# Optimization experiments

Measured on AMD Instinct MI355X. Metric: run time of the kernel, lower is better.

Reference implementation:

```python
import jax, jax.numpy as jnp
import numpy as np

N, CT, L = 8, 1024, 1024
HEADS, GROUPS = 16, 8
BN_EPS = 1e-5


def conv_bn(x, w, b, gamma, beta, mean, var, groups):
    # 1x1 grouped Conv1d followed by eval-mode BatchNorm1d.
    # x: [N, Cin, L], w: [Cout, Cin//groups], b: [Cout]
    n, cin, l = x.shape
    cout = w.shape[0]
    xg = x.reshape(n, groups, cin // groups, l)
    wg = w.reshape(groups, cout // groups, cin // groups)
    y = jnp.einsum('goi,ngil->ngol', wg, xg).reshape(n, cout, l) + b[None, :, None]
    inv = gamma / jnp.sqrt(var + BN_EPS)
    return y * inv[None, :, None] + (beta - mean * inv)[None, :, None]


def _make_params(key, cout, cin_per_group):
    ks = jax.random.split(key, 4)
    w = jax.random.normal(ks[0], (cout, cin_per_group), jnp.float32) * 0.02
    b = jnp.zeros((cout,), jnp.float32)
    gamma = jnp.ones((cout,), jnp.float32)
    beta = jnp.zeros((cout,), jnp.float32)
    mean = jax.random.normal(ks[1], (cout,), jnp.float32) * 0.1
    var = jax.random.uniform(ks[2], (cout,), jnp.float32, 0.5, 1.5)
    return w, b, gamma, beta, mean, var


def setup_inputs() -> dict:
    key = jax.random.key(0)
    k0, k1, k2, k3, k4 = jax.random.split(key, 5)
    tokens = jax.random.normal(k0, (N, CT, L), jnp.float32)
    out = {'tokens': tokens}
    for name, kk, cout, cpg in [
        ('k', k1, CT // 2, CT // GROUPS),
        ('q', k2, CT // 2, CT // GROUPS),
        ('v', k3, CT, CT // GROUPS),
        ('f', k4, CT, CT),  # ff_conv: groups=1
    ]:
        w, b, g, be, m, v = _make_params(kk, cout, cpg)
        out[f'{name}_w'], out[f'{name}_b'] = w, b
        out[f'{name}_gamma'], out[f'{name}_beta'] = g, be
        out[f'{name}_mean'], out[f'{name}_var'] = m, v
    return out


def reference(tokens,
              k_w, k_b, k_gamma, k_beta, k_mean, k_var,
              q_w, q_b, q_gamma, q_beta, q_mean, q_var,
              v_w, v_b, v_gamma, v_beta, v_mean, v_var,
              f_w, f_b, f_gamma, f_beta, f_mean, f_var):
    n, ct, l = tokens.shape
    h = HEADS
    k = conv_bn(tokens, k_w, k_b, k_gamma, k_beta, k_mean, k_var, GROUPS).reshape(n, h, ct // 2 // h, l)
    q = conv_bn(tokens, q_w, q_b, q_gamma, q_beta, q_mean, q_var, GROUPS).reshape(n, h, ct // 2 // h, l)
    v = conv_bn(tokens, v_w, v_b, v_gamma, v_beta, v_mean, v_var, GROUPS).reshape(n, h, ct // h, l)
    # kq = k^T q : [n, h, L_k, L_q]; NOTE original scales by sqrt(kq.size(2)) = sqrt(L)
    kq = jnp.einsum('nhdk,nhdq->nhkq', k, q)
    att = jax.nn.softmax(kq / jnp.sqrt(jnp.asarray(l, tokens.dtype)), axis=2)
    kqv = jnp.einsum('nhdk,nhkq->nhdq', v, att).reshape(n, ct, l)
    tokens = tokens + kqv
    tokens = tokens + conv_bn(tokens, f_w, f_b, f_gamma, f_beta, f_mean, f_var, 1)
    return tokens
```

## Files before the change

### kernel.cpp

```cpp
#include <hip/hip_runtime.h>
#include <hip/hip_bf16.h>
#include <math.h>

#define NB 8
#define BN_EPS 1e-5f
#define CEXP 0.04508422002778011f

typedef __attribute__((ext_vector_type(4))) float f32x4;
typedef __attribute__((ext_vector_type(8))) short short8;

__device__ __forceinline__ float bf2f(ushort h) {
    union { unsigned u; float f; } v; v.u = ((unsigned)h) << 16;
    return v.f;
}
__device__ __forceinline__ ushort f2bfu(float f) {
    __hip_bfloat16 h = __float2bfloat16(f);
    union { __hip_bfloat16 h; ushort u; } c; c.h = h; return c.u;
}
__device__ __forceinline__ void gld16(const ushort* g, ushort* l) {
    __builtin_amdgcn_global_load_lds(
        (const __attribute__((address_space(1))) void*)g,
        (__attribute__((address_space(3))) void*)l, 16, 0, 0);
}

#define O_WKQV   0u
#define O_BKQV   524288u
#define O_WFH    532480u
#define O_WFL    2629632u
#define O_BF     4726784u
#define O_TOKT   4730880u
#define O_T2TL   21508096u
#define O_KT     38285312u
#define O_QT     46673920u
#define O_V      55062528u
#define O_T2     71839744u

__global__ void prep_kqv(
    const float* __restrict__ kw, const float* __restrict__ kb, const float* __restrict__ kg,
    const float* __restrict__ kbe, const float* __restrict__ km, const float* __restrict__ kv,
    const float* __restrict__ qw, const float* __restrict__ qb, const float* __restrict__ qg,
    const float* __restrict__ qbe, const float* __restrict__ qm, const float* __restrict__ qv,
    const float* __restrict__ vw, const float* __restrict__ vb, const float* __restrict__ vg,
    const float* __restrict__ vbe, const float* __restrict__ vm, const float* __restrict__ vv,
    ushort* __restrict__ wf, float* __restrict__ bf)
{
    int idx = blockIdx.x * blockDim.x + threadIdx.x;
    int co = idx >> 7, ci = idx & 127;
    const float *w, *b, *g, *be, *m, *vr; int r;
    if (co < 512)       { w = kw; b = kb; g = kg; be = kbe; m = km; vr = kv; r = co; }
    else if (co < 1024) { w = qw; b = qb; g = qg; be = qbe; m = qm; vr = qv; r = co - 512; }
    else                { w = vw; b = vb; g = vg; be = vbe; m = vm; vr = vv; r = co - 1024; }
    float inv = g[r] * rsqrtf(vr[r] + BN_EPS);
    wf[idx] = f2bfu(w[r * 128 + ci] * inv);
    if (ci == 0) bf[co] = (b[r] - m[r]) * inv + be[r];
}

__global__ void prep_f(
    const float* __restrict__ fw, const float* __restrict__ fb, const float* __restrict__ fg,
    const float* __restrict__ fbe, const float* __restrict__ fm, const float* __restrict__ fv,
    ushort* __restrict__ wfh, ushort* __restrict__ wfl, float* __restrict__ bf)
{
    int idx = blockIdx.x * blockDim.x + threadIdx.x;
    int co = idx >> 10, ci = idx & 1023;
    float inv = fg[co] * rsqrtf(fv[co] + BN_EPS);
    float w = fw[idx] * inv;
    ushort hi = f2bfu(w);
    wfh[idx] = hi;
    wfl[idx] = f2bfu(w - bf2f(hi));
    if (ci == 0) bf[co] = (fb[co] - fm[co]) * inv + fbe[co];
}

__global__ __launch_bounds__(256) void transpose_tokens(
    const float* __restrict__ x, ushort* __restrict__ xt)
{
    __shared__ float Ts[64][68];
    const int l0 = blockIdx.x * 64, c0 = blockIdx.y * 64, n = blockIdx.z;
    const int tid = threadIdx.x;
    #pragma unroll
    for (int r = 0; r < 4; ++r) {
        int idx = tid + 256 * r;
        int ci = idx >> 4, li4 = (idx & 15) * 4;
        float4 v4 = *(const float4*)&x[((size_t)(n * 1024 + c0 + ci)) * 1024 + l0 + li4];
        *(float4*)&Ts[ci][li4] = v4;
    }
    __syncthreads();
    #pragma unroll
    for (int r = 0; r < 2; ++r) {
        int idx = tid + 256 * r;
        int lr = idx >> 3, oc = idx & 7;
        union { ushort u[8]; uint4 v; } pk;
        #pragma unroll
        for (int i = 0; i < 8; ++i) pk.u[i] = f2bfu(Ts[oc * 8 + i][lr]);
        *(uint4*)&xt[((size_t)(n * 1024 + l0 + lr)) * 1024 + c0 + oc * 8] = pk.v;
    }
}

__global__ __launch_bounds__(256) void conv_kqv_mfma(
    const ushort* __restrict__ xt, const ushort* __restrict__ wq,
    const float* __restrict__ bq,
    ushort* __restrict__ KT, ushort* __restrict__ QT, ushort* __restrict__ V)
{
    __shared__ ushort Ws[64 * 128];
    __shared__ ushort Xs[128 * 128];
    const int l0 = blockIdx.x * 128, co0 = blockIdx.y * 64, n = blockIdx.z;
    const int tid = threadIdx.x;
    const int wid = tid >> 6, ln = tid & 63, g = ln >> 4, ln15 = ln & 15;
    const int wm = wid >> 1, wn = wid & 1;

    int in_off;
    if (co0 < 512)       in_off = (co0 >> 6) << 7;
    else if (co0 < 1024) in_off = ((co0 - 512) >> 6) << 7;
    else                 in_off = ((co0 - 1024) >> 7) << 7;

    #pragma unroll
    for (int r = 0; r < 4; ++r) {
        int c = tid + 256 * r; int row = c >> 4, slot = c & 15;
        uint4 v4 = *(const uint4*)&wq[(size_t)(co0 + row) * 128 + slot * 8];
        *(uint4*)&Ws[row * 128 + ((slot ^ (row & 15)) << 3)] = v4;
    }
    #pragma unroll
    for (int r = 0; r < 8; ++r) {
        int c = tid + 256 * r; int row = c >> 4, slot = c & 15;
        uint4 v4 = *(const uint4*)&xt[((size_t)(n * 1024 + l0 + row)) * 1024 + in_off + slot * 8];
        *(uint4*)&Xs[row * 128 + ((slot ^ (row & 15)) << 3)] = v4;
    }
    __syncthreads();

    f32x4 acc[2][4];
    #pragma unroll
    for (int mf = 0; mf < 2; ++mf)
        #pragma unroll
        for (int nf = 0; nf < 4; ++nf) acc[mf][nf] = (f32x4){0.f, 0.f, 0.f, 0.f};

    #pragma unroll
    for (int ks = 0; ks < 4; ++ks) {
        short8 a[2], b[4];
        #pragma unroll
        for (int mf = 0; mf < 2; ++mf) {
            int row = wm * 32 + mf * 16 + ln15;
            int slot = ks * 4 + g;
            a[mf] = *(const short8*)&Ws[row * 128 + (((slot ^ (row & 15))) << 3)];
        }
        #pragma unroll
        for (int nf = 0; nf < 4; ++nf) {
            int row = wn * 64 + nf * 16 + ln15;
            int slot = ks * 4 + g;
            b[nf] = *(const short8*)&Xs[row * 128 + (((slot ^ (row & 15))) << 3)];
        }
        #pragma unroll
        for (int mf = 0; mf < 2; ++mf)
            #pragma unroll
            for (int nf = 0; nf < 4; ++nf)
                acc[mf][nf] = __builtin_amdgcn_mfma_f32_16x16x32_bf16(a[mf], b[nf], acc[mf][nf], 0, 0, 0);
    }

    #pragma unroll
    for (int mf = 0; mf < 2; ++mf) {
        int m0 = wm * 32 + mf * 16 + g * 4;
        int co = co0 + m0;
        float bb[4];
        #pragma unroll
        for (int r = 0; r < 4; ++r) bb[r] = bq[co + r];
        #pragma unroll
        for (int nf = 0; nf < 4; ++nf) {
            int l = l0 + wn * 64 + nf * 16 + ln15;
            float v0 = acc[mf][nf][0] + bb[0];
            float v1 = acc[mf][nf][1] + bb[1];
            float v2 = acc[mf][nf][2] + bb[2];
            float v3 = acc[mf][nf][3] + bb[3];
            if (co0 < 512) {
                int h = co >> 5, d = m0 & 31;
                union { ushort u[4]; uint2 v; } pk;
                pk.u[0] = f2bfu(v0); pk.u[1] = f2bfu(v1); pk.u[2] = f2bfu(v2); pk.u[3] = f2bfu(v3);
                *(uint2*)&KT[(((size_t)(n * 16 + h)) * 1024 + l) * 32 + d] = pk.v;
            } else if (co0 < 1024) {
                int cq = co - 512; int h = cq >> 5, d = m0 & 31;
                union { ushort u[4]; uint2 v; } pk;
                pk.u[0] = f2bfu(v0); pk.u[1] = f2bfu(v1); pk.u[2] = f2bfu(v2); pk.u[3] = f2bfu(v3);
                *(uint2*)&QT[(((size_t)(n * 16 + h)) * 1024 + l) * 32 + d] = pk.v;
            } else {
                int cv = co - 1024; int h = cv >> 6, dv = cv & 63;
                size_t base = (((size_t)(n * 16 + h)) * 64 + dv) * 1024 + l;
                V[base]          = f2bfu(v0);
                V[base + 1024]   = f2bfu(v1);
                V[base + 2048]   = f2bfu(v2);
                V[base + 3072]   = f2bfu(v3);
            }
        }
    }
}

__global__ __launch_bounds__(256) void attn_mfma(
    const ushort* __restrict__ KT, const ushort* __restrict__ QT, const ushort* __restrict__ V,
    const float* __restrict__ tokens, float* __restrict__ t2,
    ushort* __restrict__ t2th, ushort* __restrict__ t2tl)
{
    __shared__ ushort Vs[2][64 * 64];
    __shared__ ushort Ks[2][64 * 32];
    __shared__ ushort Pt[4][32 * 64];
    const int tid = threadIdx.x;
    const int wid = tid >> 6, ln = tid & 63, g = ln >> 4, ln15 = ln & 15;
    const int n = blockIdx.z, h = blockIdx.y;
    const int qw = blockIdx.x * 128 + wid * 32;
    const int sw7 = ln15 & 7;

    const ushort* KTh = KT + ((size_t)(n * 16 + h)) * 1024 * 32;
    const ushort* QTh = QT + ((size_t)(n * 16 + h)) * 1024 * 32;
    const ushort* Vh  = V  + ((size_t)(n * 16 + h)) * 64 * 1024;

    short8 qfr[2];
    qfr[0] = *(const short8*)&QTh[(qw + ln15) * 32 + g * 8];
    qfr[1] = *(const short8*)&QTh[(qw + 16 + ln15) * 32 + g * 8];

    const int vrow = ln >> 3, vcol = (ln & 7) ^ vrow;
    const int krow = ln >> 2, kcol = ln & 3;
    const ushort* vsrc = Vh + (size_t)(wid * 16 + vrow) * 1024 + vcol * 8;
    const ushort* ksrc = KTh + (size_t)(wid * 16 + krow) * 32 + kcol * 8;

    gld16(vsrc,            &Vs[0][wid * 1024]);
    gld16(vsrc + 8 * 1024, &Vs[0][wid * 1024 + 512]);
    gld16(ksrc,            &Ks[0][wid * 512]);
    __syncthreads();

    f32x4 acc[4][2];
    #pragma unroll
    for (int mf = 0; mf < 4; ++mf)
        #pragma unroll
        for (int qf = 0; qf < 2; ++qf) acc[mf][qf] = (f32x4){0.f, 0.f, 0.f, 0.f};
    float l_run[2] = {0.f, 0.f};
    const f32x4 zz = {0.f, 0.f, 0.f, 0.f};
    ushort* pt = &Pt[wid][0];

    for (int kt = 0; kt < 16; ++kt) {
        const int cur = kt & 1;
        if (kt < 15) {
            const int nxt = cur ^ 1;
            const int k0n = (kt + 1) * 64;
            gld16(vsrc + k0n,            &Vs[nxt][wid * 1024]);
            gld16(vsrc + k0n + 8 * 1024, &Vs[nxt][wid * 1024 + 512]);
            gld16(ksrc + k0n * 32,       &Ks[nxt][wid * 512]);
        }
        short8 kf[4];
        #pragma unroll
        for (int mf = 0; mf < 4; ++mf)
            kf[mf] = *(const short8*)&Ks[cur][(mf * 16 + ln15) * 32 + g * 8];

        #pragma unroll
        for (int qf = 0; qf < 2; ++qf) {
            f32x4 s[4];
            #pragma unroll
            for (int mf = 0; mf < 4; ++mf)
                s[mf] = __builtin_amdgcn_mfma_f32_16x16x32_bf16(kf[mf], qfr[qf], zz, 0, 0, 0);
            float lacc = 0.f;
            #pragma unroll
            for (int mf = 0; mf < 4; ++mf) {
                float p0 = __builtin_amdgcn_exp2f(s[mf][0] * CEXP);
                float p1 = __builtin_amdgcn_exp2f(s[mf][1] * CEXP);
                float p2 = __builtin_amdgcn_exp2f(s[mf][2] * CEXP);
                float p3 = __builtin_amdgcn_exp2f(s[mf][3] * CEXP);
                lacc += (p0 + p1) + (p2 + p3);
                union { ushort u[4]; uint2 v; } pk;
                pk.u[0] = f2bfu(p0); pk.u[1] = f2bfu(p1);
                pk.u[2] = f2bfu(p2); pk.u[3] = f2bfu(p3);
                *(uint2*)&pt[(qf * 16 + ln15) * 64 +
                             (((mf * 2 + (g >> 1)) ^ sw7) << 3) + (g & 1) * 4] = pk.v;
            }
            l_run[qf] += lacc;
        }

        #pragma unroll
        for (int ks = 0; ks < 2; ++ks) {
            short8 vf[4];
            #pragma unroll
            for (int mf = 0; mf < 4; ++mf)
                vf[mf] = *(const short8*)&Vs[cur][(mf * 16 + ln15) * 64 +
                                                  (((ks * 4 + g) ^ sw7) << 3)];
            #pragma unroll
            for (int qf = 0; qf < 2; ++qf) {
                short8 pf = *(const short8*)&pt[(qf * 16 + ln15) * 64 +
                                                (((ks * 4 + g) ^ sw7) << 3)];
                #pragma unroll
                for (int mf = 0; mf < 4; ++mf)
                    acc[mf][qf] = __builtin_amdgcn_mfma_f32_16x16x32_bf16(vf[mf], pf, acc[mf][qf], 0, 0, 0);
            }
        }
        __syncthreads();
    }

    #pragma unroll
    for (int qf = 0; qf < 2; ++qf) {
        float l = l_run[qf];
        l += __shfl_xor(l, 16);
        l += __shfl_xor(l, 32);
        float rl = 1.0f / l;
        const int lq = qw + qf * 16 + ln15;
        #pragma unroll
        for (int mf = 0; mf < 4; ++mf) {
            int dv = mf * 16 + g * 4;
            int c = h * 64 + dv;
            size_t base = ((size_t)(n * 1024 + c)) * 1024 + lq;
            union { ushort u[4]; uint2 v; } ph, pl;
            #pragma unroll
            for (int r = 0; r < 4; ++r) {
                float val = acc[mf][qf][r] * rl + tokens[base + (size_t)r * 1024];
                t2[base + (size_t)r * 1024] = val;
                ushort hh = f2bfu(val);
                ph.u[r] = hh;
                pl.u[r] = f2bfu(val - bf2f(hh));
            }
            size_t tb = ((size_t)(n * 1024 + lq)) * 1024 + c;
            *(uint2*)&t2th[tb] = ph.v;
            *(uint2*)&t2tl[tb] = pl.v;
        }
    }
}

__global__ __launch_bounds__(256) void conv_f_mfma(
    const ushort* __restrict__ xh, const ushort* __restrict__ xl,
    const ushort* __restrict__ wh, const ushort* __restrict__ wl,
    const float* __restrict__ bf, const float* __restrict__ t2,
    float* __restrict__ out)
{
    __shared__ ushort AsH[2][128 * 32], AsL[2][128 * 32];
    __shared__ ushort XsH[2][128 * 32], XsL[2][128 * 32];
    const int l0 = blockIdx.x * 128, co0 = blockIdx.y * 128, n = blockIdx.z;
    const int tid = threadIdx.x;
    const int wid = tid >> 6, ln = tid & 63, g = ln >> 4, ln15 = ln & 15;
    const int wm = wid >> 1, wn = wid & 1;
    const int srow = ln >> 2, scol = ln & 3;

    f32x4 acc[4][4];
    #pragma unroll
    for (int mf = 0; mf < 4; ++mf)
        #pragma unroll
        for (int nf = 0; nf < 4; ++nf) acc[mf][nf] = (f32x4){0.f, 0.f, 0.f, 0.f};

    auto stage = [&](int k0, int b) {
        #pragma unroll
        for (int j = 0; j < 2; ++j) {
            const int rr = wid * 32 + j * 16 + srow;
            const int ld = wid * 1024 + j * 512;
            const size_t wo = (size_t)(co0 + rr) * 1024 + k0 + scol * 8;
            const size_t xo = ((size_t)(n * 1024 + l0 + rr)) * 1024 + k0 + scol * 8;
            gld16(wh + wo, &AsH[b][ld]);
            gld16(wl + wo, &AsL[b][ld]);
            gld16(xh + xo, &XsH[b][ld]);
            gld16(xl + xo, &XsL[b][ld]);
        }
    };

    stage(0, 0);
    __syncthreads();

    for (int kt = 0; kt < 32; ++kt) {
        const int cur = kt & 1;
        if (kt < 31) stage((kt + 1) * 32, cur ^ 1);
        short8 ah[4], al[4], bh[4], bl[4];
        #pragma unroll
        for (int mf = 0; mf < 4; ++mf) {
            const int off = (wm * 64 + mf * 16 + ln15) * 32 + g * 8;
            ah[mf] = *(const short8*)&AsH[cur][off];
            al[mf] = *(const short8*)&AsL[cur][off];
        }
        #pragma unroll
        for (int nf = 0; nf < 4; ++nf) {
            const int off = (wn * 64 + nf * 16 + ln15) * 32 + g * 8;
            bh[nf] = *(const short8*)&XsH[cur][off];
            bl[nf] = *(const short8*)&XsL[cur][off];
        }
        #pragma unroll
        for (int mf = 0; mf < 4; ++mf)
            #pragma unroll
            for (int nf = 0; nf < 4; ++nf) {
                acc[mf][nf] = __builtin_amdgcn_mfma_f32_16x16x32_bf16(ah[mf], bh[nf], acc[mf][nf], 0, 0, 0);
                acc[mf][nf] = __builtin_amdgcn_mfma_f32_16x16x32_bf16(ah[mf], bl[nf], acc[mf][nf], 0, 0, 0);
                acc[mf][nf] = __builtin_amdgcn_mfma_f32_16x16x32_bf16(al[mf], bh[nf], acc[mf][nf], 0, 0, 0);
            }
        __syncthreads();
    }

    #pragma unroll
    for (int mf = 0; mf < 4; ++mf) {
        int co = co0 + wm * 64 + mf * 16 + g * 4;
        #pragma unroll
        for (int r = 0; r < 4; ++r) {
            float bb = bf[co + r];
            #pragma unroll
            for (int nf = 0; nf < 4; ++nf) {
                int l = l0 + wn * 64 + nf * 16 + ln15;
                size_t off = ((size_t)(n * 1024 + co + r)) * 1024 + l;
                out[off] = acc[mf][nf][r] + bb + t2[off];
            }
        }
    }
}

extern "C" void kernel_launch(void* const* d_in, const int* in_sizes, int n_in,
                              void* d_out, int out_size, void* d_ws, size_t ws_size,
                              hipStream_t stream) {
    const float* tokens = (const float*)d_in[0];
    const float* kw  = (const float*)d_in[1];
    const float* kb_ = (const float*)d_in[2];
    const float* kg  = (const float*)d_in[3];
    const float* kbe = (const float*)d_in[4];
    const float* km  = (const float*)d_in[5];
    const float* kv  = (const float*)d_in[6];
    const float* qw  = (const float*)d_in[7];
    const float* qb_ = (const float*)d_in[8];
    const float* qg  = (const float*)d_in[9];
    const float* qbe = (const float*)d_in[10];
    const float* qm  = (const float*)d_in[11];
    const float* qv  = (const float*)d_in[12];
    const float* vw  = (const float*)d_in[13];
    const float* vb_ = (const float*)d_in[14];
    const float* vg  = (const float*)d_in[15];
    const float* vbe = (const float*)d_in[16];
    const float* vm  = (const float*)d_in[17];
    const float* vv  = (const float*)d_in[18];
    const float* fw  = (const float*)d_in[19];
    const float* fb_ = (const float*)d_in[20];
    const float* fg  = (const float*)d_in[21];
    const float* fbe = (const float*)d_in[22];
    const float* fm  = (const float*)d_in[23];
    const float* fv  = (const float*)d_in[24];

    char* ws = (char*)d_ws;
    ushort* WKQV = (ushort*)(ws + O_WKQV);
    float*  BKQV = (float*)(ws + O_BKQV);
    ushort* WFH  = (ushort*)(ws + O_WFH);
    ushort* WFL  = (ushort*)(ws + O_WFL);
    float*  BF   = (float*)(ws + O_BF);
    ushort* TOKT = (ushort*)(ws + O_TOKT);
    ushort* T2TL = (ushort*)(ws + O_T2TL);
    ushort* KT   = (ushort*)(ws + O_KT);
    ushort* QT   = (ushort*)(ws + O_QT);
    ushort* Vb   = (ushort*)(ws + O_V);
    float*  T2   = (float*)(ws + O_T2);
    float*  out  = (float*)d_out;

    prep_kqv<<<1024, 256, 0, stream>>>(kw, kb_, kg, kbe, km, kv,
                                       qw, qb_, qg, qbe, qm, qv,
                                       vw, vb_, vg, vbe, vm, vv,
                                       WKQV, BKQV);
    prep_f<<<4096, 256, 0, stream>>>(fw, fb_, fg, fbe, fm, fv, WFH, WFL, BF);
    transpose_tokens<<<dim3(16, 16, NB), 256, 0, stream>>>(tokens, TOKT);
    conv_kqv_mfma<<<dim3(8, 32, NB), 256, 0, stream>>>(TOKT, WKQV, BKQV, KT, QT, Vb);
    attn_mfma<<<dim3(8, 16, NB), 256, 0, stream>>>(KT, QT, Vb, tokens, T2, TOKT, T2TL);
    conv_f_mfma<<<dim3(8, 8, NB), 256, 0, stream>>>(TOKT, T2TL, WFH, WFL, BF, T2, out);
}
```

Measured before the change: 271.9 us.

## Drop fp32 t2 buffer, fold softmax scale into Q, async LDS loads, merge prep

Merges the two weight-prep kernels into one launch and folds the softmax exponent scale into the Q weights and bias. The attention kernel now handles 64 queries per wave with a swizzled K layout, and it no longer writes the fp32 residual t2. The final conv instead rebuilds the residual from the hi/lo bf16 split already staged in LDS, adding it at the diagonal k-tile. The kqv conv switches to global_load_lds with a swizzle, and conv_f interleaves hi/lo halves in one LDS buffer. Together these cut global memory traffic and launches, at the cost of more registers per thread and a residual that is only as precise as the bf16 hi+lo pair.

```diff
diff --git a/kernel.cpp b/kernel.cpp
--- a/kernel.cpp
+++ b/kernel.cpp
@@ -33,41 +33,41 @@
 #define O_KT     38285312u
 #define O_QT     46673920u
 #define O_V      55062528u
-#define O_T2     71839744u
-
-__global__ void prep_kqv(
+
+__global__ void prep_all(
     const float* __restrict__ kw, const float* __restrict__ kb, const float* __restrict__ kg,
     const float* __restrict__ kbe, const float* __restrict__ km, const float* __restrict__ kv,
     const float* __restrict__ qw, const float* __restrict__ qb, const float* __restrict__ qg,
     const float* __restrict__ qbe, const float* __restrict__ qm, const float* __restrict__ qv,
     const float* __restrict__ vw, const float* __restrict__ vb, const float* __restrict__ vg,
     const float* __restrict__ vbe, const float* __restrict__ vm, const float* __restrict__ vv,
-    ushort* __restrict__ wf, float* __restrict__ bf)
-{
-    int idx = blockIdx.x * blockDim.x + threadIdx.x;
-    int co = idx >> 7, ci = idx & 127;
-    const float *w, *b, *g, *be, *m, *vr; int r;
-    if (co < 512)       { w = kw; b = kb; g = kg; be = kbe; m = km; vr = kv; r = co; }
-    else if (co < 1024) { w = qw; b = qb; g = qg; be = qbe; m = qm; vr = qv; r = co - 512; }
-    else                { w = vw; b = vb; g = vg; be = vbe; m = vm; vr = vv; r = co - 1024; }
-    float inv = g[r] * rsqrtf(vr[r] + BN_EPS);
-    wf[idx] = f2bfu(w[r * 128 + ci] * inv);
-    if (ci == 0) bf[co] = (b[r] - m[r]) * inv + be[r];
-}
-
-__global__ void prep_f(
     const float* __restrict__ fw, const float* __restrict__ fb, const float* __restrict__ fg,
     const float* __restrict__ fbe, const float* __restrict__ fm, const float* __restrict__ fv,
-    ushort* __restrict__ wfh, ushort* __restrict__ wfl, float* __restrict__ bf)
+    ushort* __restrict__ wkqv, float* __restrict__ bkqv,
+    ushort* __restrict__ wfh, ushort* __restrict__ wfl, float* __restrict__ bff)
 {
-    int idx = blockIdx.x * blockDim.x + threadIdx.x;
-    int co = idx >> 10, ci = idx & 1023;
-    float inv = fg[co] * rsqrtf(fv[co] + BN_EPS);
-    float w = fw[idx] * inv;
-    ushort hi = f2bfu(w);
-    wfh[idx] = hi;
-    wfl[idx] = f2bfu(w - bf2f(hi));
-    if (ci == 0) bf[co] = (fb[co] - fm[co]) * inv + fbe[co];
+    int bid = blockIdx.x;
+    int tid = threadIdx.x;
+    if (bid < 1024) {
+        int idx = bid * 256 + tid;
+        int co = idx >> 7, ci = idx & 127;
+        const float *w, *b, *g, *be, *m, *vr; int r; float sc = 1.0f;
+        if (co < 512)       { w = kw; b = kb; g = kg; be = kbe; m = km; vr = kv; r = co; }
+        else if (co < 1024) { w = qw; b = qb; g = qg; be = qbe; m = qm; vr = qv; r = co - 512; sc = CEXP; }
+        else                { w = vw; b = vb; g = vg; be = vbe; m = vm; vr = vv; r = co - 1024; }
+        float inv = g[r] * rsqrtf(vr[r] + BN_EPS) * sc;
+        wkqv[idx] = f2bfu(w[r * 128 + ci] * inv);
+        if (ci == 0) bkqv[co] = (b[r] - m[r]) * inv + be[r] * sc;
+    } else {
+        int idx = (bid - 1024) * 256 + tid;
+        int co = idx >> 10, ci = idx & 1023;
+        float inv = fg[co] * rsqrtf(fv[co] + BN_EPS);
+        float w = fw[idx] * inv;
+        ushort hi = f2bfu(w);
+        wfh[idx] = hi;
+        wfl[idx] = f2bfu(w - bf2f(hi));
+        if (ci == 0) bff[co] = (fb[co] - fm[co]) * inv + fbe[co];
+    }
 }
 
 __global__ __launch_bounds__(256) void transpose_tokens(
@@ -113,16 +113,20 @@
     else                 in_off = ((co0 - 1024) >> 7) << 7;
 
     #pragma unroll
-    for (int r = 0; r < 4; ++r) {
-        int c = tid + 256 * r; int row = c >> 4, slot = c & 15;
-        uint4 v4 = *(const uint4*)&wq[(size_t)(co0 + row) * 128 + slot * 8];
-        *(uint4*)&Ws[row * 128 + ((slot ^ (row & 15)) << 3)] = v4;
-    }
-    #pragma unroll
-    for (int r = 0; r < 8; ++r) {
-        int c = tid + 256 * r; int row = c >> 4, slot = c & 15;
-        uint4 v4 = *(const uint4*)&xt[((size_t)(n * 1024 + l0 + row)) * 1024 + in_off + slot * 8];
-        *(uint4*)&Xs[row * 128 + ((slot ^ (row & 15)) << 3)] = v4;
+    for (int j = 0; j < 4; ++j) {
+        int g16 = wid * 64 + ln + j * 256;
+        int row = g16 >> 4, phys = g16 & 15;
+        int logical = phys ^ (row & 15);
+        gld16(wq + (size_t)(co0 + row) * 128 + logical * 8,
+              &Ws[(j * 256 + wid * 64) * 8]);
+    }
+    #pragma unroll
+    for (int j = 0; j < 8; ++j) {
+        int g16 = wid * 64 + ln + j * 256;
+        int row = g16 >> 4, phys = g16 & 15;
+        int logical = phys ^ (row & 15);
+        gld16(xt + ((size_t)(n * 1024 + l0 + row)) * 1024 + in_off + logical * 8,
+              &Xs[(j * 256 + wid * 64) * 8]);
     }
     __syncthreads();
 
@@ -139,13 +143,13 @@
         for (int mf = 0; mf < 2; ++mf) {
             int row = wm * 32 + mf * 16 + ln15;
             int slot = ks * 4 + g;
-            a[mf] = *(const short8*)&Ws[row * 128 + (((slot ^ (row & 15))) << 3)];
+            a[mf] = *(const short8*)&Ws[row * 128 + ((slot ^ (row & 15)) << 3)];
         }
         #pragma unroll
         for (int nf = 0; nf < 4; ++nf) {
             int row = wn * 64 + nf * 16 + ln15;
             int slot = ks * 4 + g;
-            b[nf] = *(const short8*)&Xs[row * 128 + (((slot ^ (row & 15))) << 3)];
+            b[nf] = *(const short8*)&Xs[row * 128 + ((slot ^ (row & 15)) << 3)];
         }
         #pragma unroll
         for (int mf = 0; mf < 2; ++mf)
@@ -190,44 +194,48 @@
     }
 }
 
-__global__ __launch_bounds__(256) void attn_mfma(
+__global__ __launch_bounds__(256, 2) void attn_mfma(
     const ushort* __restrict__ KT, const ushort* __restrict__ QT, const ushort* __restrict__ V,
-    const float* __restrict__ tokens, float* __restrict__ t2,
+    const float* __restrict__ tokens,
     ushort* __restrict__ t2th, ushort* __restrict__ t2tl)
 {
     __shared__ ushort Vs[2][64 * 64];
-    __shared__ ushort Ks[2][64 * 32];
-    __shared__ ushort Pt[4][32 * 64];
+    __shared__ ushort Ks[2][32 * 64];
+    __shared__ ushort Pt[4][64 * 64];
     const int tid = threadIdx.x;
     const int wid = tid >> 6, ln = tid & 63, g = ln >> 4, ln15 = ln & 15;
     const int n = blockIdx.z, h = blockIdx.y;
-    const int qw = blockIdx.x * 128 + wid * 32;
+    const int qw = blockIdx.x * 256 + wid * 64;
     const int sw7 = ln15 & 7;
 
     const ushort* KTh = KT + ((size_t)(n * 16 + h)) * 1024 * 32;
     const ushort* QTh = QT + ((size_t)(n * 16 + h)) * 1024 * 32;
     const ushort* Vh  = V  + ((size_t)(n * 16 + h)) * 64 * 1024;
 
-    short8 qfr[2];
-    qfr[0] = *(const short8*)&QTh[(qw + ln15) * 32 + g * 8];
-    qfr[1] = *(const short8*)&QTh[(qw + 16 + ln15) * 32 + g * 8];
+    short8 qfr[4];
+    #pragma unroll
+    for (int qf = 0; qf < 4; ++qf)
+        qfr[qf] = *(const short8*)&QTh[(qw + qf * 16 + ln15) * 32 + g * 8];
 
     const int vrow = ln >> 3, vcol = (ln & 7) ^ vrow;
-    const int krow = ln >> 2, kcol = ln & 3;
     const ushort* vsrc = Vh + (size_t)(wid * 16 + vrow) * 1024 + vcol * 8;
-    const ushort* ksrc = KTh + (size_t)(wid * 16 + krow) * 32 + kcol * 8;
+    const int kgr = wid * 64 + ln;
+    const int krow = kgr >> 3, kphys = kgr & 7;
+    const int klog = kphys ^ (krow & 7);
+    const int kLocal = krow * 2 + (klog >> 2);
+    const ushort* ksrc = KTh + (size_t)kLocal * 32 + (klog & 3) * 8;
 
     gld16(vsrc,            &Vs[0][wid * 1024]);
     gld16(vsrc + 8 * 1024, &Vs[0][wid * 1024 + 512]);
     gld16(ksrc,            &Ks[0][wid * 512]);
     __syncthreads();
 
-    f32x4 acc[4][2];
+    f32x4 acc[4][4];
     #pragma unroll
     for (int mf = 0; mf < 4; ++mf)
         #pragma unroll
-        for (int qf = 0; qf < 2; ++qf) acc[mf][qf] = (f32x4){0.f, 0.f, 0.f, 0.f};
-    float l_run[2] = {0.f, 0.f};
+        for (int qf = 0; qf < 4; ++qf) acc[mf][qf] = (f32x4){0.f, 0.f, 0.f, 0.f};
+    float l_run[4] = {0.f, 0.f, 0.f, 0.f};
     const f32x4 zz = {0.f, 0.f, 0.f, 0.f};
     ushort* pt = &Pt[wid][0];
 
@@ -242,11 +250,17 @@
         }
         short8 kf[4];
         #pragma unroll
-        for (int mf = 0; mf < 4; ++mf)
-            kf[mf] = *(const short8*)&Ks[cur][(mf * 16 + ln15) * 32 + g * 8];
-
-        #pragma unroll
-        for (int qf = 0; qf < 2; ++qf) {
+        for (int mf = 0; mf < 4; ++mf) {
+            int k = mf * 16 + ln15;
+            int row = k >> 1;
+            int logical = (k & 1) * 4 + g * 2;
+            int phys = ((k & 1) * 4 + g) ^ (row & 7);
+            (void)logical;
+            kf[mf] = *(const short8*)&Ks[cur][row * 64 + phys * 8];
+        }
+
+        #pragma unroll
+        for (int qf = 0; qf < 4; ++qf) {
             f32x4 s[4];
             #pragma unroll
             for (int mf = 0; mf < 4; ++mf)
@@ -254,10 +268,10 @@
             float lacc = 0.f;
             #pragma unroll
             for (int mf = 0; mf < 4; ++mf) {
-                float p0 = __builtin_amdgcn_exp2f(s[mf][0] * CEXP);
-                float p1 = __builtin_amdgcn_exp2f(s[mf][1] * CEXP);
-                float p2 = __builtin_amdgcn_exp2f(s[mf][2] * CEXP);
-                float p3 = __builtin_amdgcn_exp2f(s[mf][3] * CEXP);
+                float p0 = __builtin_amdgcn_exp2f(s[mf][0]);
+                float p1 = __builtin_amdgcn_exp2f(s[mf][1]);
+                float p2 = __builtin_amdgcn_exp2f(s[mf][2]);
+                float p3 = __builtin_amdgcn_exp2f(s[mf][3]);
                 lacc += (p0 + p1) + (p2 + p3);
                 union { ushort u[4]; uint2 v; } pk;
                 pk.u[0] = f2bfu(p0); pk.u[1] = f2bfu(p1);
@@ -276,7 +290,7 @@
                 vf[mf] = *(const short8*)&Vs[cur][(mf * 16 + ln15) * 64 +
                                                   (((ks * 4 + g) ^ sw7) << 3)];
             #pragma unroll
-            for (int qf = 0; qf < 2; ++qf) {
+            for (int qf = 0; qf < 4; ++qf) {
                 short8 pf = *(const short8*)&pt[(qf * 16 + ln15) * 64 +
                                                 (((ks * 4 + g) ^ sw7) << 3)];
                 #pragma unroll
@@ -288,7 +302,7 @@
     }
 
     #pragma unroll
-    for (int qf = 0; qf < 2; ++qf) {
+    for (int qf = 0; qf < 4; ++qf) {
         float l = l_run[qf];
         l += __shfl_xor(l, 16);
         l += __shfl_xor(l, 32);
@@ -303,7 +317,6 @@
             #pragma unroll
             for (int r = 0; r < 4; ++r) {
                 float val = acc[mf][qf][r] * rl + tokens[base + (size_t)r * 1024];
-                t2[base + (size_t)r * 1024] = val;
                 ushort hh = f2bfu(val);
                 ph.u[r] = hh;
                 pl.u[r] = f2bfu(val - bf2f(hh));
@@ -315,19 +328,28 @@
     }
 }
 
-__global__ __launch_bounds__(256) void conv_f_mfma(
+__global__ __launch_bounds__(256, 2) void conv_f_mfma(
     const ushort* __restrict__ xh, const ushort* __restrict__ xl,
     const ushort* __restrict__ wh, const ushort* __restrict__ wl,
-    const float* __restrict__ bf, const float* __restrict__ t2,
-    float* __restrict__ out)
+    const float* __restrict__ bf, float* __restrict__ out)
 {
-    __shared__ ushort AsH[2][128 * 32], AsL[2][128 * 32];
-    __shared__ ushort XsH[2][128 * 32], XsL[2][128 * 32];
+    __shared__ ushort AHL[2][128 * 64];
+    __shared__ ushort XHL[2][128 * 64];
     const int l0 = blockIdx.x * 128, co0 = blockIdx.y * 128, n = blockIdx.z;
     const int tid = threadIdx.x;
     const int wid = tid >> 6, ln = tid & 63, g = ln >> 4, ln15 = ln & 15;
     const int wm = wid >> 1, wn = wid & 1;
-    const int srow = ln >> 2, scol = ln & 3;
+
+    const ushort* srcA[4]; const ushort* srcX[4];
+    #pragma unroll
+    for (int j = 0; j < 4; ++j) {
+        int g8 = wid * 64 + ln + j * 256;
+        int row = g8 >> 3, phys = g8 & 7;
+        int logical = phys ^ (row & 7);
+        int isLo = logical >> 2, gg = logical & 3;
+        srcA[j] = (isLo ? wl : wh) + (size_t)(co0 + row) * 1024 + gg * 8;
+        srcX[j] = (isLo ? xl : xh) + ((size_t)(n * 1024 + l0 + row)) * 1024 + gg * 8;
+    }
 
     f32x4 acc[4][4];
     #pragma unroll
@@ -337,36 +359,33 @@
 
     auto stage = [&](int k0, int b) {
         #pragma unroll
-        for (int j = 0; j < 2; ++j) {
-            const int rr = wid * 32 + j * 16 + srow;
-            const int ld = wid * 1024 + j * 512;
-            const size_t wo = (size_t)(co0 + rr) * 1024 + k0 + scol * 8;
-            const size_t xo = ((size_t)(n * 1024 + l0 + rr)) * 1024 + k0 + scol * 8;
-            gld16(wh + wo, &AsH[b][ld]);
-            gld16(wl + wo, &AsL[b][ld]);
-            gld16(xh + xo, &XsH[b][ld]);
-            gld16(xl + xo, &XsL[b][ld]);
+        for (int j = 0; j < 4; ++j) {
+            gld16(srcA[j] + k0, &AHL[b][(j * 256 + wid * 64) * 8]);
+            gld16(srcX[j] + k0, &XHL[b][(j * 256 + wid * 64) * 8]);
         }
     };
 
     stage(0, 0);
     __syncthreads();
+
+    const int kt0 = (co0 >> 5) + wm * 2;
 
     for (int kt = 0; kt < 32; ++kt) {
         const int cur = kt & 1;
         if (kt < 31) stage((kt + 1) * 32, cur ^ 1);
+
         short8 ah[4], al[4], bh[4], bl[4];
         #pragma unroll
         for (int mf = 0; mf < 4; ++mf) {
-            const int off = (wm * 64 + mf * 16 + ln15) * 32 + g * 8;
-            ah[mf] = *(const short8*)&AsH[cur][off];
-            al[mf] = *(const short8*)&AsL[cur][off];
+            const int row = wm * 64 + mf * 16 + ln15;
+            ah[mf] = *(const short8*)&AHL[cur][row * 64 + ((g       ^ (row & 7)) << 3)];
+            al[mf] = *(const short8*)&AHL[cur][row * 64 + (((4 + g) ^ (row & 7)) << 3)];
         }
         #pragma unroll
         for (int nf = 0; nf < 4; ++nf) {
-            const int off = (wn * 64 + nf * 16 + ln15) * 32 + g * 8;
-            bh[nf] = *(const short8*)&XsH[cur][off];
-            bl[nf] = *(const short8*)&XsL[cur][off];
+            const int row = wn * 64 + nf * 16 + ln15;
+            bh[nf] = *(const short8*)&XHL[cur][row * 64 + ((g       ^ (row & 7)) << 3)];
+            bl[nf] = *(const short8*)&XHL[cur][row * 64 + (((4 + g) ^ (row & 7)) << 3)];
         }
         #pragma unroll
         for (int mf = 0; mf < 4; ++mf)
@@ -376,6 +395,25 @@
                 acc[mf][nf] = __builtin_amdgcn_mfma_f32_16x16x32_bf16(ah[mf], bl[nf], acc[mf][nf], 0, 0, 0);
                 acc[mf][nf] = __builtin_amdgcn_mfma_f32_16x16x32_bf16(al[mf], bh[nf], acc[mf][nf], 0, 0, 0);
             }
+
+        if (kt == kt0 || kt == kt0 + 1) {
+            const int m0 = (kt == kt0) ? 0 : 2;
+            #pragma unroll
+            for (int mm = 0; mm < 2; ++mm) {
+                const int mf = m0 + mm;
+                const int ciG = (mf & 1) * 2 + (g >> 1);
+                const int sub = (g & 1) * 4;
+                #pragma unroll
+                for (int nf = 0; nf < 4; ++nf) {
+                    const int row = wn * 64 + nf * 16 + ln15;
+                    const ushort* ph_ = &XHL[cur][row * 64 + ((ciG       ^ (row & 7)) << 3) + sub];
+                    const ushort* pl_ = &XHL[cur][row * 64 + (((4 + ciG) ^ (row & 7)) << 3) + sub];
+                    #pragma unroll
+                    for (int r = 0; r < 4; ++r)
+                        acc[mf][nf][r] += bf2f(ph_[r]) + bf2f(pl_[r]);
+                }
+            }
+        }
         __syncthreads();
     }
 
@@ -389,7 +427,7 @@
             for (int nf = 0; nf < 4; ++nf) {
                 int l = l0 + wn * 64 + nf * 16 + ln15;
                 size_t off = ((size_t)(n * 1024 + co + r)) * 1024 + l;
-                out[off] = acc[mf][nf][r] + bb + t2[off];
+                out[off] = acc[mf][nf][r] + bb;
             }
         }
     }
@@ -435,16 +473,15 @@
     ushort* KT   = (ushort*)(ws + O_KT);
     ushort* QT   = (ushort*)(ws + O_QT);
     ushort* Vb   = (ushort*)(ws + O_V);
-    float*  T2   = (float*)(ws + O_T2);
     float*  out  = (float*)d_out;
 
-    prep_kqv<<<1024, 256, 0, stream>>>(kw, kb_, kg, kbe, km, kv,
+    prep_all<<<5120, 256, 0, stream>>>(kw, kb_, kg, kbe, km, kv,
                                        qw, qb_, qg, qbe, qm, qv,
                                        vw, vb_, vg, vbe, vm, vv,
-                                       WKQV, BKQV);
-    prep_f<<<4096, 256, 0, stream>>>(fw, fb_, fg, fbe, fm, fv, WFH, WFL, BF);
+                                       fw, fb_, fg, fbe, fm, fv,
+                                       WKQV, BKQV, WFH, WFL, BF);
     transpose_tokens<<<dim3(16, 16, NB), 256, 0, stream>>>(tokens, TOKT);
     conv_kqv_mfma<<<dim3(8, 32, NB), 256, 0, stream>>>(TOKT, WKQV, BKQV, KT, QT, Vb);
-    attn_mfma<<<dim3(8, 16, NB), 256, 0, stream>>>(KT, QT, Vb, tokens, T2, TOKT, T2TL);
-    conv_f_mfma<<<dim3(8, 8, NB), 256, 0, stream>>>(TOKT, T2TL, WFH, WFL, BF, T2, out);
-}
+    attn_mfma<<<dim3(4, 16, NB), 256, 0, stream>>>(KT, QT, Vb, tokens, TOKT, T2TL);
+    conv_f_mfma<<<dim3(8, 8, NB), 256, 0, stream>>>(TOKT, T2TL, WFH, WFL, BF, out);
+}
```

After: 500.2 us. 84.0% more time.
